# Performance work log

Measured on AMD Instinct MI355X. Metric: run time of the kernel, lower is better.

Reference implementation:

```python
import jax, jax.numpy as jnp
import numpy as np
import math

D_MODEL = 1024
NUM_HEADS = 16
D_HEAD = D_MODEL // NUM_HEADS          # 64
N_FREQ = D_HEAD // 2 + 1               # 33 rfft bins
COMPRESSION_RATIO = 0.5


def setup_inputs() -> dict:
    key = jax.random.key(0)
    k_x, k_qkv, k_out, k_b, k_m = jax.random.split(key, 5)
    B, S = 2, 2048
    x = jax.random.normal(k_x, (B, S, D_MODEL), dtype=jnp.float32)
    # Linear weights stored as [in, out] (torch Linear uses [out, in]; math identical).
    w_qkv = jax.random.normal(k_qkv, (D_MODEL, 3 * D_MODEL), dtype=jnp.float32) / math.sqrt(D_MODEL)
    w_out = jax.random.normal(k_out, (D_MODEL, D_MODEL), dtype=jnp.float32) / math.sqrt(D_MODEL)
    b_out = jax.random.normal(k_b, (D_MODEL,), dtype=jnp.float32) * 0.01
    # Learned per-frequency-bin mask logits of AdaptiveFrequencyMask(d_state=d_head).
    # Initialized around logit(compression_ratio) with small noise.
    init_logit = math.log(COMPRESSION_RATIO / (1.0 - COMPRESSION_RATIO))
    mask_logits = init_logit + 0.1 * jax.random.normal(k_m, (N_FREQ,), dtype=jnp.float32)
    return {"x": x, "w_qkv": w_qkv, "w_out": w_out, "b_out": b_out, "mask_logits": mask_logits}


def _spectral_filter(t, mask):
    # rfft over d_head dim, apply learned soft mask, inverse rfft.  t: [B,H,S,dh]
    tf = jnp.fft.rfft(t, axis=-1)          # [B,H,S,N_FREQ] complex
    tf = tf * mask                          # broadcast real mask over bins
    return jnp.fft.irfft(tf, n=t.shape[-1], axis=-1).astype(t.dtype)


def reference(x, w_qkv, w_out, b_out, mask_logits):
    B, S, D = x.shape
    H, dh = NUM_HEADS, D_HEAD
    qkv = x @ w_qkv                                         # [B,S,3D]
    q, k, v = jnp.split(qkv, 3, axis=-1)
    # [B,S,D] -> [B,H,S,dh]
    to_heads = lambda t: t.reshape(B, S, H, dh).transpose(0, 2, 1, 3)
    q, k, v = to_heads(q), to_heads(k), to_heads(v)
    mask = jax.nn.sigmoid(mask_logits)                      # [N_FREQ]
    q = _spectral_filter(q, mask)
    k = _spectral_filter(k, mask)
    scores = jnp.einsum('bhqd,bhkd->bhqk', q, k) / math.sqrt(dh)
    attn = jax.nn.softmax(scores, axis=-1)                  # dropout p=0 (eval)
    out = jnp.einsum('bhqk,bhkd->bhqd', attn, v)
    out = out.transpose(0, 2, 1, 3).reshape(B, S, D)
    return out @ w_out + b_out
```

## Files before the change

kernel.cpp:

```cpp
#include <hip/hip_runtime.h>

#define S_LEN 2048
#define NH    16
#define DH    64
#define DM    1024
#define NQKV  3072

typedef __attribute__((ext_vector_type(8))) __bf16 bf16x8;
typedef __attribute__((ext_vector_type(4))) float  f32x4;
typedef unsigned short ushort_t;

static __device__ __forceinline__ unsigned short bf16b(float f) {
  return __builtin_bit_cast(unsigned short, (__bf16)f);
}

static __device__ __forceinline__ float exp2v(float x) {
  return __builtin_amdgcn_exp2f(x);
}

static __device__ __forceinline__ bf16x8 pack8(float4 f0, float4 f1) {
  uint4 v;
  v.x = ((unsigned)bf16b(f0.y) << 16) | bf16b(f0.x);
  v.y = ((unsigned)bf16b(f0.w) << 16) | bf16b(f0.z);
  v.z = ((unsigned)bf16b(f1.y) << 16) | bf16b(f1.x);
  v.w = ((unsigned)bf16b(f1.w) << 16) | bf16b(f1.z);
  return __builtin_bit_cast(bf16x8, v);
}

static __device__ __forceinline__ void glds16(const void* g, void* l) {
  __builtin_amdgcn_global_load_lds((const __attribute__((address_space(1))) unsigned int*)g,
                                   (__attribute__((address_space(3))) unsigned int*)l, 16, 0, 0);
}

#define OFF_WT  65536ull
#define OFF_WOT 6356992ull
#define OFF_Q   8454144ull
#define OFF_K   16842752ull
#define OFF_V   25231360ull
#define OFF_AO  33619968ull

__global__ __launch_bounds__(256) void k_prep(const float* __restrict__ wqkv,
                                              const float* __restrict__ wout,
                                              const float* __restrict__ x,
                                              const float* __restrict__ logits,
                                              unsigned short* __restrict__ Wt,
                                              unsigned short* __restrict__ Wot,
                                              unsigned short* __restrict__ xb) {
  __shared__ __align__(16) char sbuf[16640];
  int bid = blockIdx.x;
  int t = threadIdx.x;

  if (bid < 256) {
    float* msk = (float*)sbuf;
    float* Kd  = (float*)(sbuf + 144);
    ushort_t (*Fb)[72] = (ushort_t(*)[72])(sbuf + 416);
    if (t < 33) msk[t] = 1.0f / (1.0f + __expf(-logits[t]));
    __syncthreads();
    if (t < 64) {
      float acc = msk[0];
      #pragma unroll
      for (int f = 1; f < 32; ++f) {
        int r = (f * t) & 63;
        acc += 2.0f * msk[f] * __cosf((float)r * (6.28318530717958647692f / 64.0f));
      }
      acc += msk[32] * ((t & 1) ? -1.0f : 1.0f);
      Kd[t] = acc * (1.0f / 64.0f);
    }
    __syncthreads();
    for (int idx = t; idx < 4096; idx += 256) {
      int j = idx >> 6, i = idx & 63;
      Fb[j][i] = bf16b(Kd[(j - i) & 63]);
    }
    __syncthreads();

    int lane = t & 63, w = t >> 6;
    int m16 = lane & 15, quad = lane >> 4;
    int kx = bid >> 5, yy = bid & 31;
    int which = yy >> 4, h = yy & 15;
    int base = which * 1024 + h * 64;

    bf16x8 af0 = *(const bf16x8*)(&Fb[w * 16 + m16][quad * 8]);
    bf16x8 af1 = *(const bf16x8*)(&Fb[w * 16 + m16][32 + quad * 8]);

    f32x4 acc[8] = {};
    #pragma unroll 2
    for (int n = 0; n < 8; ++n) {
      const float* Wg = wqkv + (size_t)(kx * 128 + n * 16 + m16) * NQKV + base + quad * 8;
      float4 a0 = *(const float4*)(Wg);
      float4 a1 = *(const float4*)(Wg + 4);
      float4 b0 = *(const float4*)(Wg + 32);
      float4 b1 = *(const float4*)(Wg + 36);
      acc[n] = __builtin_amdgcn_mfma_f32_16x16x32_bf16(af0, pack8(a0, a1), acc[n], 0, 0, 0);
      acc[n] = __builtin_amdgcn_mfma_f32_16x16x32_bf16(af1, pack8(b0, b1), acc[n], 0, 0, 0);
    }
    float sc = (which == 0) ? 0.18033688011112042f : 1.0f;
    #pragma unroll
    for (int n = 0; n < 8; ++n) {
      #pragma unroll
      for (int r = 0; r < 4; ++r) {
        int j = w * 16 + quad * 4 + r;
        Wt[(size_t)(base + j) * DM + kx * 128 + n * 16 + m16] = bf16b(acc[n][r] * sc);
      }
    }
  } else if (bid < 768) {
    float (*Ts)[65] = (float(*)[65])sbuf;
    int b1 = bid - 256;
    if (b1 < 256) {
      int kt = b1 & 15, nt = b1 >> 4;
      int cb = 2048 + nt * 64, kbase = kt * 64;
      #pragma unroll
      for (int p = 0; p < 16; ++p) {
        int kk = p * 4 + (t >> 6);
        Ts[kk][t & 63] = wqkv[(size_t)(kbase + kk) * NQKV + cb + (t & 63)];
      }
      __syncthreads();
      #pragma unroll
      for (int p = 0; p < 16; ++p) {
        int nn = p * 4 + (t >> 6);
        Wt[(size_t)(cb + nn) * DM + kbase + (t & 63)] = bf16b(Ts[t & 63][nn]);
      }
    } else {
      int b2 = b1 - 256;
      int kt = b2 & 15, nt = b2 >> 4;
      int cb = nt * 64, kbase = kt * 64;
      #pragma unroll
      for (int p = 0; p < 16; ++p) {
        int kk = p * 4 + (t >> 6);
        Ts[kk][t & 63] = wout[(size_t)(kbase + kk) * DM + cb + (t & 63)];
      }
      __syncthreads();
      #pragma unroll
      for (int p = 0; p < 16; ++p) {
        int nn = p * 4 + (t >> 6);
        Wot[(size_t)(cb + nn) * DM + kbase + (t & 63)] = bf16b(Ts[t & 63][nn]);
      }
    }
  } else {
    size_t i = ((size_t)(bid - 768) * 256 + t) * 8;
    const float4* xp = (const float4*)(x + i);
    float4 a = xp[0], b = xp[1];
    uint4 v;
    v.x = ((unsigned)bf16b(a.y) << 16) | bf16b(a.x);
    v.y = ((unsigned)bf16b(a.w) << 16) | bf16b(a.z);
    v.z = ((unsigned)bf16b(b.y) << 16) | bf16b(b.x);
    v.w = ((unsigned)bf16b(b.w) << 16) | bf16b(b.z);
    *(uint4*)(xb + i) = v;
  }
}

template<int BM, int BN, int WCOLS, int MR, int NR>
__device__ __forceinline__ void gemm_core2(const unsigned short* __restrict__ A,
                                           const unsigned short* __restrict__ Bw,
                                           int bm, int bn, unsigned short* smem,
                                           f32x4 (&acc)[MR][NR]) {
  constexpr int SLOT = (BM + BN) * 64;
  constexpr int PA = BM / 64, PB = BN / 64;
  constexpr int L = PA + PB;
  int t = threadIdx.x, lane = t & 63, w = t >> 6;
  int m16 = lane & 15, quad = lane >> 4;
  int wr = (w / WCOLS) * (MR * 16), wc = (w % WCOLS) * (NR * 16);
  int xr = m16 & 7;
  int trow = t >> 3, tcol = t & 7;
  int gsw = (tcol ^ (trow & 7)) * 8;
  const unsigned short* Ag = A  + (size_t)(bm * BM + trow) * DM + gsw;
  const unsigned short* Bg = Bw + (size_t)(bn * BN + trow) * DM + gsw;
  unsigned short* Al = smem + trow * 64 + tcol * 8;
  unsigned short* Bl = smem + BM * 64 + trow * 64 + tcol * 8;

  #pragma unroll
  for (int s = 0; s < 2; ++s) {
    #pragma unroll
    for (int p = 0; p < PA; ++p)
      glds16(Ag + (size_t)p * 64 * DM + s * 64, Al + s * SLOT + p * 4096);
    #pragma unroll
    for (int p = 0; p < PB; ++p)
      glds16(Bg + (size_t)p * 64 * DM + s * 64, Bl + s * SLOT + p * 4096);
  }

  #pragma unroll 1
  for (int ks = 0; ks < 16; ++ks) {
    if (ks < 15) asm volatile("s_waitcnt vmcnt(%0)" :: "n"(L) : "memory");
    else         asm volatile("s_waitcnt vmcnt(0)" ::: "memory");
    __builtin_amdgcn_s_barrier();
    __builtin_amdgcn_sched_barrier(0);
    const unsigned short* As = smem + (ks & 1) * SLOT;
    const unsigned short* Bs = As + BM * 64;
    #pragma unroll
    for (int kk = 0; kk < 2; ++kk) {
      bf16x8 af[MR], bfr[NR];
      #pragma unroll
      for (int i = 0; i < MR; ++i)
        af[i] = *(const bf16x8*)(As + (wr + i * 16 + m16) * 64 + ((kk * 4 + quad) ^ xr) * 8);
      #pragma unroll
      for (int j = 0; j < NR; ++j)
        bfr[j] = *(const bf16x8*)(Bs + (wc + j * 16 + m16) * 64 + ((kk * 4 + quad) ^ xr) * 8);
      #pragma unroll
      for (int i = 0; i < MR; ++i)
        #pragma unroll
        for (int j = 0; j < NR; ++j)
          acc[i][j] = __builtin_amdgcn_mfma_f32_16x16x32_bf16(af[i], bfr[j], acc[i][j], 0, 0, 0);
    }
    if (ks < 14) {
      __builtin_amdgcn_s_barrier();
      __builtin_amdgcn_sched_barrier(0);
      int kn = ks + 2;
      #pragma unroll
      for (int p = 0; p < PA; ++p)
        glds16(Ag + (size_t)p * 64 * DM + kn * 64, Al + (ks & 1) * SLOT + p * 4096);
      #pragma unroll
      for (int p = 0; p < PB; ++p)
        glds16(Bg + (size_t)p * 64 * DM + kn * 64, Bl + (ks & 1) * SLOT + p * 4096);
    }
  }
  __syncthreads();
}

__global__ __launch_bounds__(512, 1) void k_gemm_qkv(const unsigned short* __restrict__ xb,
                                                     const unsigned short* __restrict__ Bw,
                                                     unsigned short* __restrict__ Qb,
                                                     unsigned short* __restrict__ Kb,
                                                     unsigned short* __restrict__ Vt) {
  __shared__ __align__(16) unsigned short smem[65536];
  f32x4 acc[8][4] = {};
  int bid = blockIdx.x;
  int xcd = bid & 7, loc = bid >> 3;
  int bm = xcd * 2 + (loc / 12);
  int bn = loc % 12;
  gemm_core2<256, 256, 4, 8, 4>(xb, Bw, bm, bn, smem, acc);

  int t = threadIdx.x, lane = t & 63, w = t >> 6;
  int m16 = lane & 15, quad = lane >> 4;
  int b = bm >> 3, srow = (bm & 7) * 256;
  int which = bn >> 2;
  ushort_t (*Tr)[264] = (ushort_t(*)[264])smem;

  if (which < 2) {
    unsigned short* dstB = which ? Kb : Qb;
    int hbase = (bn & 3) * 4;
    #pragma unroll
    for (int ch = 0; ch < 2; ++ch) {
      if ((w >> 2) == ch) {
        #pragma unroll
        for (int i = 0; i < 8; ++i)
          #pragma unroll
          for (int j = 0; j < 4; ++j)
            #pragma unroll
            for (int r = 0; r < 4; ++r)
              Tr[i * 16 + quad * 4 + r][(w & 3) * 64 + j * 16 + m16] = bf16b(acc[i][j][r]);
      }
      __syncthreads();
      int row = t >> 2, qh = t & 3;
      unsigned short* dst = dstB +
          ((size_t)(b * 16 + hbase + qh) * 2048 + srow + ch * 128 + row) * 64;
      #pragma unroll
      for (int p = 0; p < 8; ++p)
        *(uint4*)(dst + p * 8) = *(const uint4*)(&Tr[row][qh * 64 + p * 8]);
      __syncthreads();
    }
  } else {
    int hb = (bn - 8) * 4;
    #pragma unroll
    for (int ch = 0; ch < 2; ++ch) {
      if (((w >> 1) & 1) == ch) {
        #pragma unroll
        for (int i = 0; i < 8; ++i)
          #pragma unroll
          for (int j = 0; j < 4; ++j)
            #pragma unroll
            for (int r = 0; r < 4; ++r)
              Tr[(w & 1) * 64 + j * 16 + m16][(w >> 2) * 128 + i * 16 + quad * 4 + r] =
                  bf16b(acc[i][j][r]);
      }
      __syncthreads();
      int c = t >> 2, qh = t & 3;
      int h = hb + ch * 2 + (c >> 6), d = c & 63;
      unsigned short* dst = Vt + ((size_t)(b * 16 + h) * 64 + d) * 2048 + srow;
      #pragma unroll
      for (int p = 0; p < 8; ++p)
        *(uint4*)(dst + qh * 64 + p * 8) = *(const uint4*)(&Tr[c][qh * 64 + p * 8]);
      __syncthreads();
    }
  }
}

__global__ __launch_bounds__(512, 2) void k_attn(const unsigned short* __restrict__ Qb,
                                                 const unsigned short* __restrict__ Kb,
                                                 const unsigned short* __restrict__ Vt,
                                                 unsigned short* __restrict__ AO) {
  __shared__ __align__(16) unsigned short smem[65536];
  int t = threadIdx.x;
  int w = t >> 6, lane = t & 63;
  int m16 = lane & 15, quad = lane >> 4;
  int bid = blockIdx.x;
  int jj = bid >> 3;
  int bh = ((jj & 3) << 3) + (bid & 7);
  int qbase = (jj >> 2) * 256 + w * 32;

  const unsigned short* QpA = Qb + ((size_t)bh * S_LEN + qbase + m16) * DH + quad * 8;
  const unsigned short* QpB = QpA + 16 * DH;
  bf16x8 aq0A = *(const bf16x8*)(QpA);
  bf16x8 aq1A = *(const bf16x8*)(QpA + 32);
  bf16x8 aq0B = *(const bf16x8*)(QpB);
  bf16x8 aq1B = *(const bf16x8*)(QpB + 32);
  const unsigned short* Kbase = Kb + (size_t)bh * S_LEN * DH;
  const unsigned short* Vbase = Vt + (size_t)bh * DH * S_LEN;

  int xr = m16 & 7;
  int krow0 = ((m16 >> 2) << 3) + (m16 & 3);

  int trow = t >> 3;
  int tcol = t & 7;
  int gswzK = tcol ^ ((trow & 3) | ((trow >> 1) & 4));
  int gswzV = tcol ^ (trow & 7);
  const unsigned short* Kg = Kbase + (size_t)trow * 64 + gswzK * 8;
  const unsigned short* Vg = Vbase + (size_t)trow * S_LEN + gswzV * 8;
  unsigned short* Kl = smem + trow * 64 + tcol * 8;
  unsigned short* Vl = smem + 32768 + trow * 64 + tcol * 8;

  f32x4 oA[4] = {}, oB[4] = {};
  float lA = 0.f, lB = 0.f;
  f32x4 zero = {0.f, 0.f, 0.f, 0.f};

  #pragma unroll
  for (int tt = 0; tt < 6; ++tt) {
    glds16(Kg + (size_t)tt * 4096, Kl + tt * 4096);
    glds16(Vg + tt * 64,           Vl + tt * 4096);
  }

#define QK_TILE(KSH, SA, SB)                                                              \
    _Pragma("unroll")                                                                     \
    for (int c = 0; c < 2; ++c) {                                                         \
      _Pragma("unroll")                                                                   \
      for (int gl = 0; gl < 2; ++gl) {                                                    \
        int key = c * 32 + krow0 + gl * 4;                                                \
        bf16x8 kf0 = *(const bf16x8*)((KSH) + key * 64 + ((quad ^ xr) * 8));              \
        bf16x8 kf1 = *(const bf16x8*)((KSH) + key * 64 + (((4 + quad) ^ xr) * 8));        \
        SA[c][gl] = __builtin_amdgcn_mfma_f32_16x16x32_bf16(kf0, aq0A, zero, 0, 0, 0);    \
        SA[c][gl] = __builtin_amdgcn_mfma_f32_16x16x32_bf16(kf1, aq1A, SA[c][gl], 0, 0, 0);\
        SB[c][gl] = __builtin_amdgcn_mfma_f32_16x16x32_bf16(kf0, aq0B, zero, 0, 0, 0);    \
        SB[c][gl] = __builtin_amdgcn_mfma_f32_16x16x32_bf16(kf1, aq1B, SB[c][gl], 0, 0, 0);\
      }                                                                                   \
    }

#define SM_TILE(SA, SB, PA_, PB_)                                                         \
    _Pragma("unroll")                                                                     \
    for (int c = 0; c < 2; ++c) {                                                         \
      float a0 = exp2v(SA[c][0][0]), a1 = exp2v(SA[c][0][1]);                             \
      float a2 = exp2v(SA[c][0][2]), a3 = exp2v(SA[c][0][3]);                             \
      float a4 = exp2v(SA[c][1][0]), a5 = exp2v(SA[c][1][1]);                             \
      float a6 = exp2v(SA[c][1][2]), a7 = exp2v(SA[c][1][3]);                             \
      lA += ((a0 + a1) + (a2 + a3)) + ((a4 + a5) + (a6 + a7));                            \
      uint4 ua;                                                                           \
      ua.x = ((unsigned)bf16b(a1) << 16) | bf16b(a0);                                     \
      ua.y = ((unsigned)bf16b(a3) << 16) | bf16b(a2);                                     \
      ua.z = ((unsigned)bf16b(a5) << 16) | bf16b(a4);                                     \
      ua.w = ((unsigned)bf16b(a7) << 16) | bf16b(a6);                                     \
      PA_[c] = __builtin_bit_cast(bf16x8, ua);                                            \
      float b0 = exp2v(SB[c][0][0]), b1 = exp2v(SB[c][0][1]);                             \
      float b2 = exp2v(SB[c][0][2]), b3 = exp2v(SB[c][0][3]);                             \
      float b4 = exp2v(SB[c][1][0]), b5 = exp2v(SB[c][1][1]);                             \
      float b6 = exp2v(SB[c][1][2]), b7 = exp2v(SB[c][1][3]);                             \
      lB += ((b0 + b1) + (b2 + b3)) + ((b4 + b5) + (b6 + b7));                            \
      uint4 ub;                                                                           \
      ub.x = ((unsigned)bf16b(b1) << 16) | bf16b(b0);                                     \
      ub.y = ((unsigned)bf16b(b3) << 16) | bf16b(b2);                                     \
      ub.z = ((unsigned)bf16b(b5) << 16) | bf16b(b4);                                     \
      ub.w = ((unsigned)bf16b(b7) << 16) | bf16b(b6);                                     \
      PB_[c] = __builtin_bit_cast(bf16x8, ub);                                            \
    }

#define PV_TILE(VSH, PA_, PB_)                                                            \
    _Pragma("unroll")                                                                     \
    for (int c = 0; c < 2; ++c) {                                                         \
      _Pragma("unroll")                                                                   \
      for (int j = 0; j < 4; ++j) {                                                       \
        int dv = j * 16 + m16;                                                            \
        bf16x8 bv = *(const bf16x8*)((VSH) + dv * 64 + (((c * 4 + quad) ^ xr) * 8));      \
        oA[j] = __builtin_amdgcn_mfma_f32_16x16x32_bf16(PA_[c], bv, oA[j], 0, 0, 0);      \
        oB[j] = __builtin_amdgcn_mfma_f32_16x16x32_bf16(PB_[c], bv, oB[j], 0, 0, 0);      \
      }                                                                                   \
    }

  #pragma unroll 1
  for (int wnd = 0; wnd < 16; ++wnd) {
    if (wnd < 14)      asm volatile("s_waitcnt vmcnt(8)" ::: "memory");
    else if (wnd < 15) asm volatile("s_waitcnt vmcnt(4)" ::: "memory");
    else               asm volatile("s_waitcnt vmcnt(0)" ::: "memory");
    __builtin_amdgcn_s_barrier();
    __builtin_amdgcn_sched_barrier(0);
    if (wnd < 13) {
      int ta = 2 * wnd + 6;
      glds16(Kg + (size_t)ta * 4096,       Kl + (ta & 7) * 4096);
      glds16(Vg + ta * 64,                 Vl + (ta & 7) * 4096);
      glds16(Kg + (size_t)(ta + 1) * 4096, Kl + ((ta + 1) & 7) * 4096);
      glds16(Vg + (ta + 1) * 64,           Vl + ((ta + 1) & 7) * 4096);
    }
    int s0 = (2 * wnd) & 7, s1 = (2 * wnd + 1) & 7;
    const unsigned short* Ka  = smem + s0 * 4096;
    const unsigned short* Kbs = smem + s1 * 4096;
    const unsigned short* Va  = smem + 32768 + s0 * 4096;
    const unsigned short* Vbs = smem + 32768 + s1 * 4096;

    f32x4 sA[2][2], sB[2][2];
    __builtin_amdgcn_s_setprio(1);
    QK_TILE(Ka, sA, sB)
    __builtin_amdgcn_s_setprio(0);
    bf16x8 paA[2], paB[2];
    SM_TILE(sA, sB, paA, paB)
    f32x4 tA[2][2], tB[2][2];
    __builtin_amdgcn_s_setprio(1);
    QK_TILE(Kbs, tA, tB)
    PV_TILE(Va, paA, paB)
    __builtin_amdgcn_s_setprio(0);
    bf16x8 pbA[2], pbB[2];
    SM_TILE(tA, tB, pbA, pbB)
    __builtin_amdgcn_s_setprio(1);
    PV_TILE(Vbs, pbA, pbB)
    __builtin_amdgcn_s_setprio(0);
  }
#undef QK_TILE
#undef SM_TILE
#undef PV_TILE

  lA += __shfl_xor(lA, 16); lA += __shfl_xor(lA, 32);
  lB += __shfl_xor(lB, 16); lB += __shfl_xor(lB, 32);
  float ivA = 1.0f / lA;
  float ivB = 1.0f / lB;
  int b = bh >> 4, h = bh & 15;
  #pragma unroll
  for (int r = 0; r < 4; ++r) {
    float vA = __shfl(ivA, quad * 4 + r);
    float vB = __shfl(ivB, quad * 4 + r);
    size_t row0 = (size_t)b * S_LEN + qbase + quad * 4 + r;
    unsigned short* d0 = AO + row0 * DM + h * DH + m16;
    unsigned short* d1 = AO + (row0 + 16) * DM + h * DH + m16;
    #pragma unroll
    for (int j = 0; j < 4; ++j) {
      d0[j * 16] = bf16b(oA[j][r] * vA);
      d1[j * 16] = bf16b(oB[j][r] * vB);
    }
  }
}

__global__ __launch_bounds__(512, 1) void k_gemm_out(const unsigned short* __restrict__ A,
                                                     const unsigned short* __restrict__ Bw,
                                                     const float* __restrict__ bias,
                                                     float* __restrict__ out) {
  __shared__ __align__(16) unsigned short smem[32768];
  f32x4 acc[4][2] = {};
  int bid = blockIdx.x;
  int xcd = bid & 7, loc = bid >> 3;
  int bm = xcd * 4 + (loc >> 3);
  int bn = loc & 7;
  gemm_core2<128, 128, 4, 4, 2>(A, Bw, bm, bn, smem, acc);

  int t = threadIdx.x, lane = t & 63, w = t >> 6;
  int m16 = lane & 15, quad = lane >> 4;
  int wr = (w >> 2) * 64, wc = (w & 3) * 32;
  #pragma unroll
  for (int i = 0; i < 4; ++i) {
    int grow = bm * 128 + wr + i * 16 + quad * 4;
    #pragma unroll
    for (int j = 0; j < 2; ++j) {
      int gc = bn * 128 + wc + j * 16 + m16;
      float bb = bias[gc];
      #pragma unroll
      for (int r = 0; r < 4; ++r)
        out[(size_t)(grow + r) * DM + gc] = acc[i][j][r] + bb;
    }
  }
}

extern "C" void kernel_launch(void* const* d_in, const int* in_sizes, int n_in,
                              void* d_out, int out_size, void* d_ws, size_t ws_size,
                              hipStream_t stream) {
  const float* x    = (const float*)d_in[0];
  const float* wqkv = (const float*)d_in[1];
  const float* wout = (const float*)d_in[2];
  const float* bout = (const float*)d_in[3];
  const float* mlog = (const float*)d_in[4];
  char* ws = (char*)d_ws;
  unsigned short* Wt  = (unsigned short*)(ws + OFF_WT);
  unsigned short* Wot = (unsigned short*)(ws + OFF_WOT);
  unsigned short* Qb  = (unsigned short*)(ws + OFF_Q);
  unsigned short* Kb  = (unsigned short*)(ws + OFF_K);
  unsigned short* Vt  = (unsigned short*)(ws + OFF_V);
  unsigned short* xb  = (unsigned short*)(ws + OFF_AO);
  unsigned short* AO  = (unsigned short*)(ws + OFF_AO);
  float* out = (float*)d_out;

  k_prep<<<dim3(2816), dim3(256), 0, stream>>>(wqkv, wout, x, mlog, Wt, Wot, xb);
  k_gemm_qkv<<<dim3(192), dim3(512), 0, stream>>>(xb, Wt, Qb, Kb, Vt);
  k_attn<<<dim3(256), dim3(512), 0, stream>>>(Qb, Kb, Vt, AO);
  k_gemm_out<<<dim3(256), dim3(512), 0, stream>>>(AO, Wot, bout, out);
}
```

Measured before the change: 183.7 us.

## Use 128x128 tiles with 4-stage pipelined core for QKV GEMM

```diff
diff --git a/kernel.cpp b/kernel.cpp
--- a/kernel.cpp
+++ b/kernel.cpp
@@ -146,6 +146,76 @@
     v.w = ((unsigned)bf16b(b.w) << 16) | bf16b(b.z);
     *(uint4*)(xb + i) = v;
   }
+}
+
+__device__ __forceinline__ void gemm_core4_128(const unsigned short* __restrict__ A,
+                                               const unsigned short* __restrict__ Bw,
+                                               int bm, int bn, unsigned short* smem,
+                                               f32x4 (&acc)[4][2]) {
+  constexpr int SLOT = 256 * 64;
+  int t = threadIdx.x, lane = t & 63, w = t >> 6;
+  int m16 = lane & 15, quad = lane >> 4;
+  int wr = (w >> 2) * 64, wc = (w & 3) * 32;
+  int xr = m16 & 7;
+
+  const unsigned short* Ag[2];
+  const unsigned short* Bg[2];
+  unsigned short* Al[2];
+  unsigned short* Bl[2];
+  #pragma unroll
+  for (int j = 0; j < 2; ++j) {
+    int ca = t + j * 512;
+    int row = ca >> 3, tcol = ca & 7;
+    int gsw = (tcol ^ (row & 7)) * 8;
+    Ag[j] = A  + (size_t)(bm * 128 + row) * DM + gsw;
+    Bg[j] = Bw + (size_t)(bn * 128 + row) * DM + gsw;
+    Al[j] = smem + ca * 8;
+    Bl[j] = smem + 8192 + ca * 8;
+  }
+
+  #pragma unroll
+  for (int s = 0; s < 3; ++s) {
+    #pragma unroll
+    for (int j = 0; j < 2; ++j) {
+      glds16(Ag[j] + s * 64, Al[j] + s * SLOT);
+      glds16(Bg[j] + s * 64, Bl[j] + s * SLOT);
+    }
+  }
+
+  #pragma unroll 1
+  for (int ks = 0; ks < 16; ++ks) {
+    if (ks < 14)      asm volatile("s_waitcnt vmcnt(8)" ::: "memory");
+    else if (ks < 15) asm volatile("s_waitcnt vmcnt(4)" ::: "memory");
+    else              asm volatile("s_waitcnt vmcnt(0)" ::: "memory");
+    __builtin_amdgcn_s_barrier();
+    __builtin_amdgcn_sched_barrier(0);
+    if (ks < 13) {
+      int ta = ks + 3, sl = ta & 3;
+      #pragma unroll
+      for (int j = 0; j < 2; ++j) {
+        glds16(Ag[j] + ta * 64, Al[j] + sl * SLOT);
+        glds16(Bg[j] + ta * 64, Bl[j] + sl * SLOT);
+      }
+    }
+    const unsigned short* As = smem + (ks & 3) * SLOT;
+    const unsigned short* Bs = As + 8192;
+    #pragma unroll
+    for (int kk = 0; kk < 2; ++kk) {
+      bf16x8 af[4], bfr[2];
+      #pragma unroll
+      for (int i = 0; i < 4; ++i)
+        af[i] = *(const bf16x8*)(As + (wr + i * 16 + m16) * 64 + ((kk * 4 + quad) ^ xr) * 8);
+      #pragma unroll
+      for (int j = 0; j < 2; ++j)
+        bfr[j] = *(const bf16x8*)(Bs + (wc + j * 16 + m16) * 64 + ((kk * 4 + quad) ^ xr) * 8);
+      #pragma unroll
+      for (int i = 0; i < 4; ++i)
+        #pragma unroll
+        for (int j = 0; j < 2; ++j)
+          acc[i][j] = __builtin_amdgcn_mfma_f32_16x16x32_bf16(af[i], bfr[j], acc[i][j], 0, 0, 0);
+    }
+  }
+  __syncthreads();
 }
 
 template<int BM, int BN, int WCOLS, int MR, int NR>
@@ -221,65 +291,53 @@
                                                      unsigned short* __restrict__ Kb,
                                                      unsigned short* __restrict__ Vt) {
   __shared__ __align__(16) unsigned short smem[65536];
-  f32x4 acc[8][4] = {};
+  f32x4 acc[4][2] = {};
   int bid = blockIdx.x;
   int xcd = bid & 7, loc = bid >> 3;
-  int bm = xcd * 2 + (loc / 12);
-  int bn = loc % 12;
-  gemm_core2<256, 256, 4, 8, 4>(xb, Bw, bm, bn, smem, acc);
+  int bm = xcd * 4 + (loc / 24);
+  int bn = loc % 24;
+  gemm_core4_128(xb, Bw, bm, bn, smem, acc);
 
   int t = threadIdx.x, lane = t & 63, w = t >> 6;
   int m16 = lane & 15, quad = lane >> 4;
-  int b = bm >> 3, srow = (bm & 7) * 256;
-  int which = bn >> 2;
-  ushort_t (*Tr)[264] = (ushort_t(*)[264])smem;
+  int wr = (w >> 2) * 64, wc = (w & 3) * 32;
+  int b = bm >> 4, srow = (bm & 15) * 128;
+  int cb = bn * 128;
+  int which = cb >> 10;
+  int h0 = (cb >> 6) & 15;
+  ushort_t (*Tr)[132] = (ushort_t(*)[132])smem;
 
   if (which < 2) {
-    unsigned short* dstB = which ? Kb : Qb;
-    int hbase = (bn & 3) * 4;
-    #pragma unroll
-    for (int ch = 0; ch < 2; ++ch) {
-      if ((w >> 2) == ch) {
+    #pragma unroll
+    for (int i = 0; i < 4; ++i)
+      #pragma unroll
+      for (int j = 0; j < 2; ++j)
         #pragma unroll
-        for (int i = 0; i < 8; ++i)
-          #pragma unroll
-          for (int j = 0; j < 4; ++j)
-            #pragma unroll
-            for (int r = 0; r < 4; ++r)
-              Tr[i * 16 + quad * 4 + r][(w & 3) * 64 + j * 16 + m16] = bf16b(acc[i][j][r]);
-      }
-      __syncthreads();
-      int row = t >> 2, qh = t & 3;
-      unsigned short* dst = dstB +
-          ((size_t)(b * 16 + hbase + qh) * 2048 + srow + ch * 128 + row) * 64;
-      #pragma unroll
-      for (int p = 0; p < 8; ++p)
-        *(uint4*)(dst + p * 8) = *(const uint4*)(&Tr[row][qh * 64 + p * 8]);
-      __syncthreads();
-    }
+        for (int r = 0; r < 4; ++r)
+          Tr[wr + i * 16 + quad * 4 + r][wc + j * 16 + m16] = bf16b(acc[i][j][r]);
+    __syncthreads();
+    int row = t >> 2, qh = t & 3;
+    int h = h0 + (qh >> 1);
+    unsigned short* dst = (which ? Kb : Qb) +
+        ((size_t)(b * 16 + h) * 2048 + srow + row) * 64 + (qh & 1) * 32;
+    #pragma unroll
+    for (int p = 0; p < 4; ++p)
+      *(uint4*)(dst + p * 8) = *(const uint4*)(&Tr[row][qh * 32 + p * 8]);
   } else {
-    int hb = (bn - 8) * 4;
-    #pragma unroll
-    for (int ch = 0; ch < 2; ++ch) {
-      if (((w >> 1) & 1) == ch) {
+    #pragma unroll
+    for (int i = 0; i < 4; ++i)
+      #pragma unroll
+      for (int j = 0; j < 2; ++j)
         #pragma unroll
-        for (int i = 0; i < 8; ++i)
-          #pragma unroll
-          for (int j = 0; j < 4; ++j)
-            #pragma unroll
-            for (int r = 0; r < 4; ++r)
-              Tr[(w & 1) * 64 + j * 16 + m16][(w >> 2) * 128 + i * 16 + quad * 4 + r] =
-                  bf16b(acc[i][j][r]);
-      }
-      __syncthreads();
-      int c = t >> 2, qh = t & 3;
-      int h = hb + ch * 2 + (c >> 6), d = c & 63;
-      unsigned short* dst = Vt + ((size_t)(b * 16 + h) * 64 + d) * 2048 + srow;
-      #pragma unroll
-      for (int p = 0; p < 8; ++p)
-        *(uint4*)(dst + qh * 64 + p * 8) = *(const uint4*)(&Tr[c][qh * 64 + p * 8]);
-      __syncthreads();
-    }
+        for (int r = 0; r < 4; ++r)
+          Tr[wc + j * 16 + m16][wr + i * 16 + quad * 4 + r] = bf16b(acc[i][j][r]);
+    __syncthreads();
+    int c = t >> 2, qh = t & 3;
+    int h = h0 + (c >> 6), d = c & 63;
+    unsigned short* dst = Vt + ((size_t)(b * 16 + h) * 64 + d) * 2048 + srow + qh * 32;
+    #pragma unroll
+    for (int p = 0; p < 4; ++p)
+      *(uint4*)(dst + p * 8) = *(const uint4*)(&Tr[c][qh * 32 + p * 8]);
   }
 }
 
@@ -490,7 +548,7 @@
   float* out = (float*)d_out;
 
   k_prep<<<dim3(2816), dim3(256), 0, stream>>>(wqkv, wout, x, mlog, Wt, Wot, xb);
-  k_gemm_qkv<<<dim3(192), dim3(512), 0, stream>>>(xb, Wt, Qb, Kb, Vt);
+  k_gemm_qkv<<<dim3(768), dim3(512), 0, stream>>>(xb, Wt, Qb, Kb, Vt);
   k_attn<<<dim3(256), dim3(512), 0, stream>>>(Qb, Kb, Vt, AO);
   k_gemm_out<<<dim3(256), dim3(512), 0, stream>>>(AO, Wot, bout, out);
 }
```

Result: no change. 184.8 us (+0.6%).
